# Performance work log

Hardware: AMD Instinct MI355X
Metric: run time of the kernel (lower is better)

The kernel has to match this reference:

```python
import jax, jax.numpy as jnp
import numpy as np


def setup_inputs() -> dict:
    key = jax.random.key(0)
    k1, k2 = jax.random.split(key)
    pred_corners = jax.random.normal(k1, (2048, 8, 3), dtype=jnp.float32)
    gt_corners = jax.random.normal(k2, (2048, 8, 3), dtype=jnp.float32)
    return {"pred_corners": pred_corners, "gt_corners": gt_corners}


def _chamfer(pred_corners, gt_corners):
    # flatten boxes -> point clouds: [Np*8, 3], [Ng*8, 3]
    x = pred_corners.reshape(-1, 3)
    y = gt_corners.reshape(-1, 3)
    x2 = jnp.sum(x * x, axis=-1)  # [N]
    y2 = jnp.sum(y * y, axis=-1)  # [M]
    d2 = x2[:, None] + y2[None, :] - 2.0 * jnp.einsum("nd,md->nm", x, y)
    dist = jnp.sqrt(jnp.maximum(d2, 0.0))  # [N, M]
    # bidirectional min, averaged per box (8 corners) then over boxes
    min_p2g = jnp.min(dist, axis=1).reshape(-1, 8).mean(axis=1)
    min_g2p = jnp.min(dist, axis=0).reshape(-1, 8).mean(axis=1)
    return min_p2g.mean() + min_g2p.mean()


def reference(pred_corners, gt_corners):
    return _chamfer(pred_corners, gt_corners)
```

## Files before the change

### kernel.cpp

```cpp
#include <hip/hip_runtime.h>


#define NPTS   16384
#define BLOCK  256
#define XCH    256
#define NXC    (NPTS / XCH)
#define YW     128
#define YCH    (4 * YW)
#define NYC    (NPTS / YCH)
#define ONEBF  0x3F80

#define WS_PGB  (1u << 20)
#define WS_PART (2u << 20)
#define NROWSL  NYC
#define NCOLSL  NXC

typedef __attribute__((ext_vector_type(8))) short bf16x8;
typedef __attribute__((ext_vector_type(4))) float f32x4;

__device__ inline unsigned short f2bf(float f) {
    unsigned int u = __float_as_uint(f);
    return (unsigned short)((u + 0x7FFFu + ((u >> 16) & 1u)) >> 16);
}
__device__ inline float bf2f(unsigned short h) {
    return __uint_as_float((unsigned int)h << 16);
}
__device__ inline void split3(float v, unsigned short* s) {
    unsigned short h = f2bf(v);  float r = v - bf2f(h);
    unsigned short m = f2bf(r);  r -= bf2f(m);
    s[0] = h; s[1] = m; s[2] = f2bf(r);
}

__device__ inline void build_rows(const float p[3], unsigned short* a,
                                  unsigned short* b) {
    const int CI[6] = {0, 0, 1, 0, 1, 2};
    const int CJ[6] = {0, 1, 0, 2, 1, 0};
    unsigned short xs[3][3], nn[3], t[3];
#pragma unroll
    for (int d = 0; d < 3; ++d) {
        split3(p[d], t);
        xs[0][d] = t[0]; xs[1][d] = t[1]; xs[2][d] = t[2];
    }
    split3(-0.5f * (p[0]*p[0] + p[1]*p[1] + p[2]*p[2]), nn);
#pragma unroll
    for (int c = 0; c < 6; ++c)
#pragma unroll
        for (int d = 0; d < 3; ++d) {
            a[c*3+d] = xs[CI[c]][d];
            b[c*3+d] = xs[CJ[c]][d];
        }
#pragma unroll
    for (int k = 0; k < 3; ++k) {
        a[18+k] = nn[k];  b[18+k] = ONEBF;
        a[21+k] = ONEBF;  b[21+k] = nn[k];
    }
#pragma unroll
    for (int k = 24; k < 32; ++k) { a[k] = 0; b[k] = 0; }
}

__device__ inline void store_row(unsigned short* dst, const unsigned short* s) {
    unsigned int w[16];
#pragma unroll
    for (int k = 0; k < 16; ++k)
        w[k] = (unsigned int)s[2*k] | ((unsigned int)s[2*k+1] << 16);
    uint4* d4 = reinterpret_cast<uint4*>(dst);
#pragma unroll
    for (int k = 0; k < 4; ++k)
        d4[k] = make_uint4(w[4*k], w[4*k+1], w[4*k+2], w[4*k+3]);
}

__global__ __launch_bounds__(256) void pack_points(
        const float* __restrict__ pred, const float* __restrict__ gt,
        unsigned short* __restrict__ Ppa, unsigned short* __restrict__ Pgb,
        float* __restrict__ out) {
    const int i = blockIdx.x * 256 + threadIdx.x;
    if (i == 0) out[0] = 0.0f;
    if (i >= NPTS) return;
    float p[3] = {pred[3*i], pred[3*i+1], pred[3*i+2]};
    float q[3] = {gt[3*i],   gt[3*i+1],   gt[3*i+2]};
    unsigned short ra[32], rb[32];
    build_rows(p, ra, rb);
    store_row(Ppa + (size_t)i * 32, ra);
    build_rows(q, ra, rb);
    store_row(Pgb + (size_t)i * 32, rb);
}

template <int CTRL>
__device__ inline float rormax(float v) {
    int t = __builtin_amdgcn_update_dpp(0, __float_as_int(v), CTRL, 0xF, 0xF,
                                        false);
    return fmaxf(v, __int_as_float(t));
}

__global__ __launch_bounds__(BLOCK)
__attribute__((amdgpu_waves_per_eu(2, 4)))
void chamfer_bidi(
        const unsigned short* __restrict__ Ppa,
        const unsigned short* __restrict__ Pgb,
        float* __restrict__ part) {
    const int yc = blockIdx.x;
    const int xb = blockIdx.y;
    const int tid = threadIdx.x;
    const int lane = tid & 63, w = tid >> 6;
    const int col = lane & 15, kg = lane >> 4;
    const int xbase = xb * XCH;
    const int ybase = yc * YCH + w * YW;

    __shared__ __align__(16) unsigned short Ash[XCH * 32];
    __shared__ float rowacc[4][XCH];

    {
        const uint4* src = reinterpret_cast<const uint4*>(Ppa + (size_t)xbase * 32);
        uint4* dst = reinterpret_cast<uint4*>(Ash);
#pragma unroll
        for (int j = 0; j < 4; ++j)
            dst[j * 256 + tid] = src[j * 256 + tid];
    }

    bf16x8 bfr[8];
#pragma unroll
    for (int yt = 0; yt < 8; ++yt)
        bfr[yt] = *reinterpret_cast<const bf16x8*>(
            Pgb + (size_t)(ybase + yt * 16 + col) * 32 + kg * 8);

    float cmax[8];
#pragma unroll
    for (int yt = 0; yt < 8; ++yt) cmax[yt] = -3.0e38f;

    const f32x4 z4 = {0.0f, 0.0f, 0.0f, 0.0f};

    __syncthreads();

#pragma unroll 1
    for (int xt = 0; xt < 16; ++xt) {
        bf16x8 afc = *reinterpret_cast<const bf16x8*>(
            Ash + (xt * 16 + col) * 32 + kg * 8);

        f32x4 rmax = {-3.0e38f, -3.0e38f, -3.0e38f, -3.0e38f};
#pragma unroll
        for (int yt = 0; yt < 8; yt += 2) {
            f32x4 A = __builtin_amdgcn_mfma_f32_16x16x32_bf16(afc, bfr[yt],     z4, 0, 0, 0);
            f32x4 B = __builtin_amdgcn_mfma_f32_16x16x32_bf16(afc, bfr[yt + 1], z4, 0, 0, 0);
            rmax.x = fmaxf(fmaxf(A.x, B.x), rmax.x);
            rmax.y = fmaxf(fmaxf(A.y, B.y), rmax.y);
            rmax.z = fmaxf(fmaxf(A.z, B.z), rmax.z);
            rmax.w = fmaxf(fmaxf(A.w, B.w), rmax.w);
            float ta = fmaxf(fmaxf(A.x, A.y), A.z);
            cmax[yt]     = fmaxf(fmaxf(ta, A.w), cmax[yt]);
            float tb = fmaxf(fmaxf(B.x, B.y), B.z);
            cmax[yt + 1] = fmaxf(fmaxf(tb, B.w), cmax[yt + 1]);
        }

#pragma unroll
        for (int i = 0; i < 4; ++i) {
            float v = rmax[i];
            v = rormax<0x121>(v);
            v = rormax<0x122>(v);
            v = rormax<0x124>(v);
            v = rormax<0x128>(v);
            if (col == 0)
                rowacc[w][xt * 16 + kg * 4 + i] = fmaxf(-2.0f * v, 0.0f);
        }
    }

#pragma unroll
    for (int yt = 0; yt < 8; ++yt) {
        float v = cmax[yt];
        v = fmaxf(v, __shfl_xor(v, 16, 64));
        v = fmaxf(v, __shfl_xor(v, 32, 64));
        if (kg == 0)
            part[(size_t)(NROWSL + xb) * NPTS + ybase + yt * 16 + col] =
                fmaxf(-2.0f * v, 0.0f);
    }

    __syncthreads();
    float m = fminf(fminf(rowacc[0][tid], rowacc[1][tid]),
                    fminf(rowacc[2][tid], rowacc[3][tid]));
    part[(size_t)yc * NPTS + xbase + tid] = m;
}

__global__ __launch_bounds__(256) void chamfer_reduce(
        const float* __restrict__ part, float* __restrict__ out) {
    const int gid = blockIdx.x * 256 + threadIdx.x;
    const int side = gid >> 12;
    const int idx4 = (gid & 4095) * 4;
    const int off  = side ? NROWSL : 0;
    const int cnt  = side ? NCOLSL : NROWSL;
    float4 m = make_float4(3.0e38f, 3.0e38f, 3.0e38f, 3.0e38f);
#pragma unroll 8
    for (int c = 0; c < cnt; ++c) {
        float4 v = *reinterpret_cast<const float4*>(
            part + (size_t)(off + c) * NPTS + idx4);
        m.x = fminf(m.x, v.x); m.y = fminf(m.y, v.y);
        m.z = fminf(m.z, v.z); m.w = fminf(m.w, v.w);
    }
    float s = sqrtf(m.x) + sqrtf(m.y) + sqrtf(m.z) + sqrtf(m.w);
#pragma unroll
    for (int o = 32; o > 0; o >>= 1)
        s += __shfl_down(s, o, 64);
    if ((threadIdx.x & 63) == 0)
        atomicAdd(out, s * (1.0f / (float)NPTS));
}

extern "C" void kernel_launch(void* const* d_in, const int* in_sizes, int n_in,
                              void* d_out, int out_size, void* d_ws, size_t ws_size,
                              hipStream_t stream) {
    const float* pred = (const float*)d_in[0];
    const float* gt   = (const float*)d_in[1];
    float* out        = (float*)d_out;
    unsigned short* Ppa = (unsigned short*)d_ws;
    unsigned short* Pgb = (unsigned short*)((char*)d_ws + WS_PGB);
    float* part         = (float*)((char*)d_ws + WS_PART);

    hipLaunchKernelGGL(pack_points, dim3(NPTS / 256), dim3(256), 0, stream,
                       pred, gt, Ppa, Pgb, out);
    hipLaunchKernelGGL(chamfer_bidi, dim3(NYC, NXC), dim3(BLOCK), 0, stream,
                       Ppa, Pgb, part);
    hipLaunchKernelGGL(chamfer_reduce, dim3(2 * NPTS / 1024), dim3(256), 0, stream,
                       part, out);
}
```

Measured before the change: 96.00 us.

## Retile chamfer kernel: share gt tiles in LDS, keep pred fragments in registers

The main kernel's tiling is inverted. Each block now loads a 128-point gt chunk into LDS, shared by all four waves, while each wave keeps four 16-point pred fragments in registers and writes its row partial minima straight to global memory. Pack_points now stores the operands in a fragment-swizzled order so each lane's MFMA load is a contiguous uint4. The change also drops the waves_per_eu hint and uses a small LDS max-combine for the column minima. In exchange the grid has four times as many, smaller blocks. The row-partial buffer grows from 32 to 128 slices, which raises reduce-kernel traffic and workspace use.

```diff
diff --git a/kernel.cpp b/kernel.cpp
--- a/kernel.cpp
+++ b/kernel.cpp
@@ -3,17 +3,17 @@
 
 #define NPTS   16384
 #define BLOCK  256
+#define XW     64
 #define XCH    256
-#define NXC    (NPTS / XCH)
-#define YW     128
-#define YCH    (4 * YW)
+#define NXB    (NPTS / XCH)
+#define YCH    128
 #define NYC    (NPTS / YCH)
 #define ONEBF  0x3F80
 
 #define WS_PGB  (1u << 20)
 #define WS_PART (2u << 20)
 #define NROWSL  NYC
-#define NCOLSL  NXC
+#define NCOLSL  NXB
 
 typedef __attribute__((ext_vector_type(8))) short bf16x8;
 typedef __attribute__((ext_vector_type(4))) float f32x4;
@@ -58,15 +58,16 @@
     for (int k = 24; k < 32; ++k) { a[k] = 0; b[k] = 0; }
 }
 
-__device__ inline void store_row(unsigned short* dst, const unsigned short* s) {
+__device__ inline void store_row_swz(uint4* dst4, int i, const unsigned short* s) {
     unsigned int w[16];
 #pragma unroll
     for (int k = 0; k < 16; ++k)
         w[k] = (unsigned int)s[2*k] | ((unsigned int)s[2*k+1] << 16);
-    uint4* d4 = reinterpret_cast<uint4*>(dst);
-#pragma unroll
-    for (int k = 0; k < 4; ++k)
-        d4[k] = make_uint4(w[4*k], w[4*k+1], w[4*k+2], w[4*k+3]);
+    const int base = (i >> 4) * 64 + (i & 15);
+#pragma unroll
+    for (int kgc = 0; kgc < 4; ++kgc)
+        dst4[base + kgc * 16] = make_uint4(w[4*kgc], w[4*kgc+1],
+                                           w[4*kgc+2], w[4*kgc+3]);
 }
 
 __global__ __launch_bounds__(256) void pack_points(
@@ -80,9 +81,9 @@
     float q[3] = {gt[3*i],   gt[3*i+1],   gt[3*i+2]};
     unsigned short ra[32], rb[32];
     build_rows(p, ra, rb);
-    store_row(Ppa + (size_t)i * 32, ra);
+    store_row_swz(reinterpret_cast<uint4*>(Ppa), i, ra);
     build_rows(q, ra, rb);
-    store_row(Pgb + (size_t)i * 32, rb);
+    store_row_swz(reinterpret_cast<uint4*>(Pgb), i, rb);
 }
 
 template <int CTRL>
@@ -92,9 +93,7 @@
     return fmaxf(v, __int_as_float(t));
 }
 
-__global__ __launch_bounds__(BLOCK)
-__attribute__((amdgpu_waves_per_eu(2, 4)))
-void chamfer_bidi(
+__global__ __launch_bounds__(BLOCK) void chamfer_bidi(
         const unsigned short* __restrict__ Ppa,
         const unsigned short* __restrict__ Pgb,
         float* __restrict__ part) {
@@ -103,26 +102,28 @@
     const int tid = threadIdx.x;
     const int lane = tid & 63, w = tid >> 6;
     const int col = lane & 15, kg = lane >> 4;
-    const int xbase = xb * XCH;
-    const int ybase = yc * YCH + w * YW;
-
-    __shared__ __align__(16) unsigned short Ash[XCH * 32];
-    __shared__ float rowacc[4][XCH];
+    const int frag = kg * 16 + col;
+
+    __shared__ uint4 Bsh[YCH * 4];
+    __shared__ float colacc[4][YCH];
 
     {
-        const uint4* src = reinterpret_cast<const uint4*>(Ppa + (size_t)xbase * 32);
-        uint4* dst = reinterpret_cast<uint4*>(Ash);
-#pragma unroll
-        for (int j = 0; j < 4; ++j)
-            dst[j * 256 + tid] = src[j * 256 + tid];
-    }
-
-    bf16x8 bfr[8];
-#pragma unroll
-    for (int yt = 0; yt < 8; ++yt)
-        bfr[yt] = *reinterpret_cast<const bf16x8*>(
-            Pgb + (size_t)(ybase + yt * 16 + col) * 32 + kg * 8);
-
+        const uint4* bsrc = reinterpret_cast<const uint4*>(Pgb) + yc * (YCH * 4);
+        Bsh[tid]       = bsrc[tid];
+        Bsh[256 + tid] = bsrc[256 + tid];
+    }
+
+    const uint4* ap = reinterpret_cast<const uint4*>(Ppa);
+    const int tile0 = xb * 16 + w * 4;
+    bf16x8 af[4];
+#pragma unroll
+    for (int xi = 0; xi < 4; ++xi)
+        af[xi] = *reinterpret_cast<const bf16x8*>(&ap[(tile0 + xi) * 64 + frag]);
+
+    f32x4 rmax[4];
+#pragma unroll
+    for (int xi = 0; xi < 4; ++xi)
+        rmax[xi] = (f32x4){-3.0e38f, -3.0e38f, -3.0e38f, -3.0e38f};
     float cmax[8];
 #pragma unroll
     for (int yt = 0; yt < 8; ++yt) cmax[yt] = -3.0e38f;
@@ -132,34 +133,36 @@
     __syncthreads();
 
 #pragma unroll 1
-    for (int xt = 0; xt < 16; ++xt) {
-        bf16x8 afc = *reinterpret_cast<const bf16x8*>(
-            Ash + (xt * 16 + col) * 32 + kg * 8);
-
-        f32x4 rmax = {-3.0e38f, -3.0e38f, -3.0e38f, -3.0e38f};
-#pragma unroll
-        for (int yt = 0; yt < 8; yt += 2) {
-            f32x4 A = __builtin_amdgcn_mfma_f32_16x16x32_bf16(afc, bfr[yt],     z4, 0, 0, 0);
-            f32x4 B = __builtin_amdgcn_mfma_f32_16x16x32_bf16(afc, bfr[yt + 1], z4, 0, 0, 0);
-            rmax.x = fmaxf(fmaxf(A.x, B.x), rmax.x);
-            rmax.y = fmaxf(fmaxf(A.y, B.y), rmax.y);
-            rmax.z = fmaxf(fmaxf(A.z, B.z), rmax.z);
-            rmax.w = fmaxf(fmaxf(A.w, B.w), rmax.w);
+    for (int yt = 0; yt < 8; yt += 2) {
+        bf16x8 b0 = *reinterpret_cast<const bf16x8*>(&Bsh[(yt + 0) * 64 + frag]);
+        bf16x8 b1 = *reinterpret_cast<const bf16x8*>(&Bsh[(yt + 1) * 64 + frag]);
+#pragma unroll
+        for (int xi = 0; xi < 4; ++xi) {
+            f32x4 A = __builtin_amdgcn_mfma_f32_16x16x32_bf16(af[xi], b0, z4, 0, 0, 0);
+            f32x4 B = __builtin_amdgcn_mfma_f32_16x16x32_bf16(af[xi], b1, z4, 0, 0, 0);
+            rmax[xi].x = fmaxf(fmaxf(A.x, B.x), rmax[xi].x);
+            rmax[xi].y = fmaxf(fmaxf(A.y, B.y), rmax[xi].y);
+            rmax[xi].z = fmaxf(fmaxf(A.z, B.z), rmax[xi].z);
+            rmax[xi].w = fmaxf(fmaxf(A.w, B.w), rmax[xi].w);
             float ta = fmaxf(fmaxf(A.x, A.y), A.z);
             cmax[yt]     = fmaxf(fmaxf(ta, A.w), cmax[yt]);
             float tb = fmaxf(fmaxf(B.x, B.y), B.z);
             cmax[yt + 1] = fmaxf(fmaxf(tb, B.w), cmax[yt + 1]);
         }
-
-#pragma unroll
-        for (int i = 0; i < 4; ++i) {
-            float v = rmax[i];
+    }
+
+    float* rowp = part + (size_t)yc * NPTS + xb * XCH + w * XW;
+#pragma unroll
+    for (int xi = 0; xi < 4; ++xi) {
+#pragma unroll
+        for (int c = 0; c < 4; ++c) {
+            float v = rmax[xi][c];
             v = rormax<0x121>(v);
             v = rormax<0x122>(v);
             v = rormax<0x124>(v);
             v = rormax<0x128>(v);
             if (col == 0)
-                rowacc[w][xt * 16 + kg * 4 + i] = fmaxf(-2.0f * v, 0.0f);
+                rowp[xi * 16 + kg * 4 + c] = fmaxf(-2.0f * v, 0.0f);
         }
     }
 
@@ -168,15 +171,15 @@
         float v = cmax[yt];
         v = fmaxf(v, __shfl_xor(v, 16, 64));
         v = fmaxf(v, __shfl_xor(v, 32, 64));
-        if (kg == 0)
-            part[(size_t)(NROWSL + xb) * NPTS + ybase + yt * 16 + col] =
-                fmaxf(-2.0f * v, 0.0f);
-    }
-
+        if (kg == 0) colacc[w][yt * 16 + col] = v;
+    }
     __syncthreads();
-    float m = fminf(fminf(rowacc[0][tid], rowacc[1][tid]),
-                    fminf(rowacc[2][tid], rowacc[3][tid]));
-    part[(size_t)yc * NPTS + xbase + tid] = m;
+    if (tid < YCH) {
+        float v = fmaxf(fmaxf(colacc[0][tid], colacc[1][tid]),
+                        fmaxf(colacc[2][tid], colacc[3][tid]));
+        part[(size_t)(NROWSL + xb) * NPTS + yc * YCH + tid] =
+            fmaxf(-2.0f * v, 0.0f);
+    }
 }
 
 __global__ __launch_bounds__(256) void chamfer_reduce(
@@ -214,7 +217,7 @@
 
     hipLaunchKernelGGL(pack_points, dim3(NPTS / 256), dim3(256), 0, stream,
                        pred, gt, Ppa, Pgb, out);
-    hipLaunchKernelGGL(chamfer_bidi, dim3(NYC, NXC), dim3(BLOCK), 0, stream,
+    hipLaunchKernelGGL(chamfer_bidi, dim3(NYC, NXB), dim3(BLOCK), 0, stream,
                        Ppa, Pgb, part);
     hipLaunchKernelGGL(chamfer_reduce, dim3(2 * NPTS / 1024), dim3(256), 0, stream,
                        part, out);
```

Result: slower. 118.7 us (+23.6%).
